# Kernel optimization log

Hardware: AMD Instinct MI355X
Metric: run time of the kernel (lower is better)

## Reference

```python
import jax, jax.numpy as jnp
import numpy as np

L = 2048   # input_len
D = 768    # d_model
K = 24     # num_eigh
K_U = 3    # auto_reg_k_u
K_Y = 2    # auto_reg_k_y


def get_top_hankel_eigh(n, k):
    # Hankel matrix Z[i,j] = 2 / ((i+j)^3 - (i+j)), 1-indexed
    i = np.arange(1, n + 1, dtype=np.float64)
    s = i[:, None] + i[None, :]
    z = 2.0 / (s ** 3 - s)
    vals, vecs = np.linalg.eigh(z)
    return (jnp.asarray(vals[-k:], jnp.float32),      # [k]
            jnp.asarray(vecs[:, -k:], jnp.float32))   # [n, k]


def setup_inputs() -> dict:
    key = jax.random.key(0)
    k1, k2, k3, k4 = jax.random.split(key, 4)
    inputs = jax.random.normal(k1, (L, D), jnp.float32)
    m_y = 0.01 * jax.random.normal(k2, (D, K_Y, D), jnp.float32)
    m_u = (1.0 / D ** 0.5) * jax.random.normal(k3, (D, D, K_U), jnp.float32)
    m_phi = 0.02 * jax.random.normal(k4, (D * K, D), jnp.float32)
    eig_vals, eig_vecs = get_top_hankel_eigh(L, K)
    return {"inputs": inputs, "m_y": m_y, "m_u": m_u, "m_phi": m_phi,
            "eig_vals": eig_vals, "eig_vecs": eig_vecs}


def _conv(v, u):
    # Causal (truncated) convolution of every filter with every channel via FFT.
    # v: [l, k] spectral filters, u: [l, d] inputs -> [l, k, d]
    l = v.shape[0]
    vf = jnp.fft.rfft(v, n=2 * l, axis=0)   # [l+1, k]
    uf = jnp.fft.rfft(u, n=2 * l, axis=0)   # [l+1, d]
    return jnp.fft.irfft(vf[:, :, None] * uf[:, None, :], n=2 * l, axis=0)[:l]


def _compute_x_tilde(inputs, eig_vals, eig_vecs, do_shift=True):
    l = inputs.shape[0]
    x = _conv(eig_vecs, inputs) * (eig_vals[None, :, None] ** 0.25)  # [l, k, d]
    x = x.reshape(l, -1)                                             # [l, k*d]
    if do_shift:
        # shift twice (zero-pad at front); the first two lags are handled by AR part
        x = jnp.pad(x, ((2, 0), (0, 0)))[:l]
    return x


def _compute_ar_x_preds(w, x):
    # w: [d_out, d_in, k_u], x: [l, d_in] -> [l, d_out]
    d_out, d_in, k = w.shape
    l = x.shape[0]
    o = jnp.einsum('oik,li->klo', w, x)                     # [k, l, d_out]
    o = jax.vmap(lambda a, s: jnp.roll(a, s, axis=0))(o, jnp.arange(k))
    m = jnp.triu(jnp.ones((k, l), dtype=x.dtype))[:, :, None]  # zero wrap-around
    return jnp.sum(o * m, axis=0)


def _compute_y_t(m_y, deltas):
    # y_t = sum_i m_y[:, i] @ y_{t-1-i} + delta_t, as a linear recurrence scan
    d_out, k, _ = m_y.shape

    def step(carry, x):                                 # carry: [k, d_out]
        out = jnp.tensordot(m_y, carry, axes=2) + x     # [d_out]
        carry = jnp.concatenate([out[None], carry[:-1]], axis=0)
        return carry, out

    _, ys = jax.lax.scan(step, jnp.zeros((k, d_out), deltas.dtype), deltas)
    return ys


def reference(inputs, m_y, m_u, m_phi, eig_vals, eig_vecs):
    x_tilde = _compute_x_tilde(inputs, eig_vals, eig_vecs, True)  # [l, k*d]
    delta_phi = x_tilde @ m_phi                                   # [l, d]
    delta_ar_u = _compute_ar_x_preds(m_u, inputs)                 # [l, d]
    return _compute_y_t(m_y, delta_phi + delta_ar_u)              # [l, d]
```

## Files before the change

kernel.cpp:

```cpp
#include <hip/hip_runtime.h>
#include <hip/hip_bf16.h>
#include <stdint.h>


typedef unsigned short u16;
typedef unsigned int   u32;
typedef __bf16  bf16x8 __attribute__((ext_vector_type(8)));
typedef float   f32x4  __attribute__((ext_vector_type(4)));
typedef u32     u32x4  __attribute__((ext_vector_type(4)));

#define MFMA(a,b,c) __builtin_amdgcn_mfma_f32_16x16x32_bf16(a,b,c,0,0,0)
#define RJ 1179648

__device__ __forceinline__ u16 f2b(float f) {
  union { float f; u32 u; } v; v.f = f;
  return (u16)((v.u + 0x7fffu + ((v.u >> 16) & 1u)) >> 16);
}

__device__ __forceinline__ void gld16(const u16* g, u16* l) {
  __builtin_amdgcn_global_load_lds(
      (const __attribute__((address_space(1))) u32*)g,
      (__attribute__((address_space(3))) u32*)l, 16, 0, 0);
}

#define WS_UB     0
#define WS_MPHIT  3148800
#define WS_B2T    31460352
#define WS_TT     34999296
#define WS_ZT     48368640
#define WS_DELTA  123866112
#define OV_RBIG   (WS_ZT + 0)
#define OV_CT0    (WS_ZT + 21233664)
#define OV_CT1    (WS_ZT + 25952256)
#define OV_CT2    (WS_ZT + 30670848)
#define OV_HBUF   (WS_ZT + 35389440)
#define OV_SBUF   (WS_ZT + 41680896)

__global__ void k_prep(const float* __restrict__ u, const float* __restrict__ mphi,
                       const float* __restrict__ ev, const float* __restrict__ mu,
                       const float* __restrict__ evec,
                       float* __restrict__ delta, u16* __restrict__ ub,
                       u16* __restrict__ mphiT, u16* __restrict__ b2t,
                       u16* __restrict__ tt) {
  __shared__ float tile[32][33];
  int b = blockIdx.x, tid = threadIdx.x;
  if (b < 6144) {
    delta[b * 256 + tid] = 0.f;
  } else if (b < 12294) {
    int i = (b - 6144) * 256 + tid;
    ub[i] = (i < 2 * 768) ? (u16)0 : f2b(u[i - 2 * 768]);
  } else if (b < 26118) {
    int bid = b - 12294;
    int k = bid / 576, rem = bid % 576;
    int ti = rem / 24, tj = rem % 24;
    int c = tid & 31, r0 = tid >> 5;
    float s = powf(ev[k], 0.25f);
    #pragma unroll
    for (int rr = 0; rr < 4; ++rr) {
      int r = r0 + (rr << 3);
      tile[r][c] = mphi[(k * 768 + ti * 32 + r) * 768 + tj * 32 + c];
    }
    __syncthreads();
    #pragma unroll
    for (int rr = 0; rr < 4; ++rr) {
      int r = r0 + (rr << 3);
      mphiT[(k * 768 + tj * 32 + r) * 768 + ti * 32 + c] = f2b(tile[c][r] * s);
    }
  } else if (b < 33030) {
    int i = (b - 26118) * 256 + tid;
    int kk = i / (768 * 768);
    int rem = i % (768 * 768);
    int o = rem / 768, ii = rem % 768;
    b2t[i] = f2b(mu[(o * 768 + ii) * 3 + kk]);
  } else {
    int i = (b - 33030) * 256 + tid;
    int c = i & 127, r = (i >> 7) & 127;
    int kk = (i >> 14) % 24, sl = (i >> 14) / 24;
    int t = (sl - 1) * 128 + r - c - 2;
    tt[i] = (t >= 0 && t < 2048) ? f2b(evec[t * 24 + kk]) : (u16)0;
  }
}

__device__ __forceinline__ void stage128(const u16* __restrict__ g, int ld,
                                         u16* __restrict__ lds) {
  int tid = threadIdx.x;
  int r0 = tid >> 3, cb = tid & 7, wave = tid >> 6;
  #pragma unroll
  for (int s = 0; s < 4; ++s) {
    int row = r0 + (s << 5);
    int cbx = (cb ^ (row & 7)) << 3;
    gld16(g + row * ld + cbx, lds + (s << 11) + (wave << 9));
  }
}

__device__ __forceinline__ void mfma_tile(const u16* As, const u16* Bs, int lane,
                                          int wm, int wn, f32x4 acc[4][4]) {
  int cn = lane & 15, q = lane >> 4;
  #pragma unroll
  for (int ks = 0; ks < 2; ++ks) {
    int blk = ks * 4 + q;
    bf16x8 af[4], bg[4];
    #pragma unroll
    for (int i = 0; i < 4; ++i) {
      int row = wm + i * 16 + cn;
      af[i] = *(const bf16x8*)&As[row * 64 + ((blk ^ (row & 7)) << 3)];
    }
    #pragma unroll
    for (int j = 0; j < 4; ++j) {
      int row = wn + j * 16 + cn;
      bg[j] = *(const bf16x8*)&Bs[row * 64 + ((blk ^ (row & 7)) << 3)];
    }
    #pragma unroll
    for (int i = 0; i < 4; ++i)
      #pragma unroll
      for (int j = 0; j < 4; ++j)
        acc[i][j] = MFMA(af[i], bg[j], acc[i][j]);
  }
}

__device__ __forceinline__ void mfma_tile256(const u16* As, const u16* Bs, int lane,
                                             int wm, f32x4 acc[4][8]) {
  int cn = lane & 15, q = lane >> 4;
  #pragma unroll
  for (int ks = 0; ks < 2; ++ks) {
    int blk = ks * 4 + q;
    bf16x8 af[4], bg[8];
    #pragma unroll
    for (int i = 0; i < 4; ++i) {
      int row = wm + i * 16 + cn;
      af[i] = *(const bf16x8*)&As[row * 64 + ((blk ^ (row & 7)) << 3)];
    }
    #pragma unroll
    for (int j = 0; j < 8; ++j) {
      int row = j * 16 + cn;
      bg[j] = *(const bf16x8*)&Bs[row * 64 + ((blk ^ (row & 7)) << 3)];
    }
    #pragma unroll
    for (int i = 0; i < 4; ++i)
      #pragma unroll
      for (int j = 0; j < 8; ++j)
        acc[i][j] = MFMA(af[i], bg[j], acc[i][j]);
  }
}

__global__ __launch_bounds__(256, 2) void k_gemm_zt(const u16* __restrict__ A,
                                                    const u16* __restrict__ B,
                                                    u16* __restrict__ C) {
  __shared__ __align__(16) u16 As[256 * 64];
  __shared__ __align__(16) u16 Bs[128 * 64];
  int bid = blockIdx.x;
  bid = (bid & 7) * 144 + (bid >> 3);
  int nt = bid & 15, mt = bid >> 4;
  int m0 = mt << 8, n0 = nt << 7;
  int tid = threadIdx.x, lane = tid & 63, wave = tid >> 6;
  int wm = wave << 6;
  f32x4 acc[4][8] = {};
  for (int kb = 0; kb < 12; ++kb) {
    stage128(A + m0 * 768 + kb * 64, 768, As);
    stage128(A + (m0 + 128) * 768 + kb * 64, 768, As + 8192);
    stage128(B + n0 * 768 + kb * 64, 768, Bs);
    __syncthreads();
    mfma_tile256(As, Bs, lane, wm, acc);
    __syncthreads();
  }
  int q = lane >> 4, cn = lane & 15;
  #pragma unroll
  for (int i = 0; i < 4; ++i)
    #pragma unroll
    for (int j = 0; j < 8; ++j)
      #pragma unroll
      for (int r = 0; r < 4; ++r) {
        int m = m0 + wm + i * 16 + q * 4 + r;
        int n = n0 + j * 16 + cn;
        C[m * 2048 + n] = f2b(acc[i][j][r]);
      }
}

__global__ __launch_bounds__(256, 2) void k_gemm_delta(const u16* __restrict__ tt,
                                                       const u16* __restrict__ zt,
                                                       const u16* __restrict__ ub,
                                                       const u16* __restrict__ b2t,
                                                       float* __restrict__ delta) {
  __shared__ __align__(16) u16 As[256 * 64];
  __shared__ __align__(16) u16 Bs[128 * 64];
  int bid = blockIdx.x;
  bid = (bid & 7) * 54 + (bid >> 3);
  int s = 0, rem = bid;
  for (;; ++s) { int c = 6 * (8 - (s >> 1)); if (rem < c) break; rem -= c; }
  int cnt = 8 - (s >> 1);
  int db = rem / cnt;
  int a  = (s >> 1) + rem % cnt;
  int n0 = db << 7;
  int tid = threadIdx.x, lane = tid & 63, wave = tid >> 6;
  int wm = wave << 6;
  f32x4 acc[4][8] = {};
  int d1 = 2 * a + 1 - s;
  const u16* A0 = tt + (size_t)d1 * 24 * 16384;
  const u16* A1 = tt + (size_t)(d1 + 1) * 24 * 16384;
  for (int kk = 0; kk < 24; ++kk) {
    const u16* Bg = zt + kk * (768 * 2048) + n0 * 2048 + s * 128;
    #pragma unroll
    for (int hf = 0; hf < 2; ++hf) {
      stage128(A0 + kk * 16384 + hf * 64, 128, As);
      stage128(A1 + kk * 16384 + hf * 64, 128, As + 8192);
      stage128(Bg + hf * 64, 2048, Bs);
      __syncthreads();
      mfma_tile256(As, Bs, lane, wm, acc);
      __syncthreads();
    }
  }
  #pragma unroll
  for (int kku = 0; kku < 3; ++kku) {
    int owner = (kku <= 2 * a + 1) ? kku : 2 * a + 1;
    if (s != owner) continue;
    const u16* Au = ub + (2 + a * 256 - kku) * 768;
    const u16* Bg = b2t + kku * (768 * 768) + n0 * 768;
    for (int ic = 0; ic < 12; ++ic) {
      stage128(Au + ic * 64, 768, As);
      stage128(Au + 128 * 768 + ic * 64, 768, As + 8192);
      stage128(Bg + ic * 64, 768, Bs);
      __syncthreads();
      mfma_tile256(As, Bs, lane, wm, acc);
      __syncthreads();
    }
  }
  int q = lane >> 4, cn = lane & 15;
  #pragma unroll
  for (int i = 0; i < 4; ++i)
    #pragma unroll
    for (int j = 0; j < 8; ++j)
      #pragma unroll
      for (int r = 0; r < 4; ++r) {
        int m = a * 256 + wm + i * 16 + q * 4 + r;
        int n = n0 + j * 16 + cn;
        unsafeAtomicAdd(&delta[m * 768 + n], acc[i][j][r]);
      }
}

__global__ void k_chain_init(const float* __restrict__ my, u16* __restrict__ Rbig,
                             u16* __restrict__ Ct0, u16* __restrict__ Ct1,
                             float* __restrict__ Hbuf) {
  int b = blockIdx.x, tid = threadIdx.x;
  if (b < 4608) {
    int i = b * 256 + tid;
    int o = i / 1536, q = i % 1536;
    Rbig[i] = (q == o) ? (u16)0x3F80 : (u16)0;
    Rbig[RJ + i] = f2b(my[i]);
  } else if (b < 13824) {
    int i = (b - 4608) * 256 + tid;
    int n = i / 1536, p = i % 1536;
    u16 v;
    if (p < 768) v = f2b(my[p * 1536 + n]);
    else         v = (p - 768 == n) ? (u16)0x3F80 : (u16)0;
    Ct0[i] = v;
  } else if (b < 18432) {
    int i = (b - 13824) * 256 + tid;
    int n = i / 768, ii = i % 768;
    Ct1[n * 1536 + 768 + ii] = f2b(my[ii * 1536 + n]);
  } else {
    int i = (b - 18432) * 256 + tid;
    Hbuf[i] = 0.f;
  }
}

__global__ __launch_bounds__(256) void k_gemm_R(const u16* __restrict__ A,
                                                const u16* __restrict__ Ct,
                                                u16* __restrict__ Co,
                                                u16* __restrict__ CtT, int mode) {
  __shared__ __align__(16) u16 As[128 * 64];
  __shared__ __align__(16) u16 Bs[128 * 64];
  int bid = blockIdx.x;
  int nt = bid % 12, mt = bid / 12;
  int m0 = mt << 7, n0 = nt << 7;
  int tid = threadIdx.x, lane = tid & 63, wave = tid >> 6;
  int wm = (wave & 1) << 6, wn = (wave >> 1) << 6;
  f32x4 acc[4][4] = {};
  for (int kb = 0; kb < 24; ++kb) {
    stage128(A + m0 * 1536 + kb * 64, 1536, As);
    stage128(Ct + n0 * 1536 + kb * 64, 1536, Bs);
    __syncthreads();
    mfma_tile(As, Bs, lane, wm, wn, acc);
    __syncthreads();
  }
  int q = lane >> 4, cn = lane & 15;
  #pragma unroll
  for (int i = 0; i < 4; ++i)
    #pragma unroll
    for (int j = 0; j < 4; ++j) {
      int n = n0 + wn + j * 16 + cn;
      int mb = m0 + wm + i * 16 + q * 4;
      u16 pk[4];
      #pragma unroll
      for (int r = 0; r < 4; ++r) {
        u16 v = f2b(acc[i][j][r]);
        Co[(mb + r) * 1536 + n] = v;
        pk[r] = v;
      }
      if (mode) {
        int tcol = (mode == 1) ? mb : ((mb < 768) ? 768 + mb : mb - 768);
        *(uint2*)&CtT[n * 1536 + tcol] = *(uint2*)pk;
      }
    }
}

__global__ __launch_bounds__(256) void k_conv(const float* __restrict__ delta,
                                              const u16* __restrict__ Rbig,
                                              float* __restrict__ Hbuf) {
  __shared__ __align__(16) u16 As[128 * 64];
  __shared__ __align__(16) u16 Bs[128 * 64];
  int bid = blockIdx.x;
  bid = (bid & 7) * 48 + (bid >> 3);
  int nt = bid % 6, mt = (bid / 6) % 16, sp = bid / 96;
  int m0 = mt << 7, n0 = nt << 7;
  int tid = threadIdx.x, lane = tid & 63, wave = tid >> 6;
  int wm = (wave & 1) << 6, wn = (wave >> 1) << 6;
  int trow = tid >> 3, cb = tid & 7;
  f32x4 acc[4][4] = {};
  for (int kb = 0; kb < 24; ++kb) {
    int i = 2 * sp + kb / 12, dinb = kb % 12;
    #pragma unroll
    for (int s = 0; s < 4; ++s) {
      int row = trow + (s << 5);
      int t = m0 + row;
      u16 pk[8] = {0, 0, 0, 0, 0, 0, 0, 0};
      if (i <= (t & 7)) {
        const float* src = delta + (t - i) * 768 + dinb * 64 + (cb << 3);
        f32x4 v0 = *(const f32x4*)src;
        f32x4 v1 = *(const f32x4*)(src + 4);
        #pragma unroll
        for (int e = 0; e < 4; ++e) { pk[e] = f2b(v0[e]); pk[4 + e] = f2b(v1[e]); }
      }
      *(u32x4*)&As[row * 64 + ((cb ^ (row & 7)) << 3)] = *(u32x4*)pk;
    }
    stage128(Rbig + i * RJ + n0 * 1536 + dinb * 64, 1536, Bs);
    __syncthreads();
    mfma_tile(As, Bs, lane, wm, wn, acc);
    __syncthreads();
  }
  int q = lane >> 4, cn = lane & 15;
  #pragma unroll
  for (int i = 0; i < 4; ++i)
    #pragma unroll
    for (int j = 0; j < 4; ++j)
      #pragma unroll
      for (int r = 0; r < 4; ++r) {
        int m = m0 + wm + i * 16 + q * 4 + r;
        int n = n0 + wn + j * 16 + cn;
        unsafeAtomicAdd(&Hbuf[m * 768 + n], acc[i][j][r]);
      }
}

__global__ __launch_bounds__(256) void k_scan_roundA(const u16* __restrict__ Rbig,
                                                     const float* __restrict__ Hbuf,
                                                     u16* __restrict__ Sout) {
  __shared__ __align__(16) u16 As[128 * 64];
  __shared__ __align__(16) u16 Bs[128 * 64];
  int bid = blockIdx.x;
  int nt = bid % 12, mt = bid / 12;
  int m0 = mt << 7, n0 = nt << 7;
  const u16* Bg = (nt < 6) ? (Rbig + 8 * RJ + n0 * 1536)
                           : (Rbig + 7 * RJ + (n0 - 768) * 1536);
  int tid = threadIdx.x, lane = tid & 63, wave = tid >> 6;
  int wm = (wave & 1) << 6, wn = (wave >> 1) << 6;
  int trow = tid >> 3, cb = tid & 7;
  f32x4 acc[4][4] = {};
  for (int kb = 0; kb < 24; ++kb) {
    #pragma unroll
    for (int s = 0; s < 4; ++s) {
      int row = trow + (s << 5);
      int c = m0 + row;
      int qb = kb * 64 + (cb << 3);
      int side = (qb >= 768) ? 1 : 0;
      int o0 = qb - side * 768;
      int t = 8 * c - 17 - side;
      u16 pk[8] = {0, 0, 0, 0, 0, 0, 0, 0};
      if (t >= 0) {
        const float* src = Hbuf + t * 768 + o0;
        f32x4 v0 = *(const f32x4*)src;
        f32x4 v1 = *(const f32x4*)(src + 4);
        #pragma unroll
        for (int e = 0; e < 4; ++e) { pk[e] = f2b(v0[e]); pk[4 + e] = f2b(v1[e]); }
      }
      *(u32x4*)&As[row * 64 + ((cb ^ (row & 7)) << 3)] = *(u32x4*)pk;
    }
    stage128(Bg + kb * 64, 1536, Bs);
    __syncthreads();
    mfma_tile(As, Bs, lane, wm, wn, acc);
    __syncthreads();
  }
  int q = lane >> 4, cn = lane & 15;
  #pragma unroll
  for (int i = 0; i < 4; ++i)
    #pragma unroll
    for (int j = 0; j < 4; ++j)
      #pragma unroll
      for (int r = 0; r < 4; ++r) {
        int c = m0 + wm + i * 16 + q * 4 + r;
        int n = n0 + wn + j * 16 + cn;
        int side = (n < 768) ? 0 : 1;
        int t = 8 * c - 9 - side;
        int o = n - side * 768;
        float val = acc[i][j][r] + ((t >= 0) ? Hbuf[t * 768 + o] : 0.f);
        Sout[c * 1536 + n] = f2b(val);
      }
}

__global__ __launch_bounds__(256) void k_scan_round(const u16* __restrict__ Sin,
                                                    const u16* __restrict__ Rbig,
                                                    const float* __restrict__ Hbuf,
                                                    u16* __restrict__ Sout) {
  __shared__ __align__(16) u16 As[128 * 64];
  __shared__ __align__(16) u16 Bs[128 * 64];
  int bid = blockIdx.x;
  int nt = bid % 12, mt = bid / 12;
  int m0 = mt << 7, n0 = nt << 7;
  const u16* Bg = (nt < 6) ? (Rbig + 8 * RJ + n0 * 1536)
                           : (Rbig + 7 * RJ + (n0 - 768) * 1536);
  int tid = threadIdx.x, lane = tid & 63, wave = tid >> 6;
  int wm = (wave & 1) << 6, wn = (wave >> 1) << 6;
  f32x4 acc[4][4] = {};
  for (int kb = 0; kb < 24; ++kb) {
    stage128(Sin + m0 * 1536 + kb * 64, 1536, As);
    stage128(Bg + kb * 64, 1536, Bs);
    __syncthreads();
    mfma_tile(As, Bs, lane, wm, wn, acc);
    __syncthreads();
  }
  int q = lane >> 4, cn = lane & 15;
  #pragma unroll
  for (int i = 0; i < 4; ++i)
    #pragma unroll
    for (int j = 0; j < 4; ++j)
      #pragma unroll
      for (int r = 0; r < 4; ++r) {
        int c = m0 + wm + i * 16 + q * 4 + r;
        int n = n0 + wn + j * 16 + cn;
        int side = (n < 768) ? 0 : 1;
        int t = 8 * c - 1 - side;
        int o = n - side * 768;
        float val = acc[i][j][r] + ((t >= 0) ? Hbuf[t * 768 + o] : 0.f);
        Sout[c * 1536 + n] = f2b(val);
      }
}

__global__ __launch_bounds__(256) void k_scan_out(const u16* __restrict__ Sin,
                                                  const u16* __restrict__ Rbig,
                                                  const float* __restrict__ Hbuf,
                                                  float* __restrict__ out) {
  __shared__ __align__(16) u16 As[128 * 64];
  __shared__ __align__(16) u16 Bs[128 * 64];
  int bid = blockIdx.x;
  int nt = bid % 48, mt = bid / 48;
  int m0 = mt << 7, n0 = nt << 7;
  const u16* Bg = Rbig + RJ + n0 * 1536;
  int tid = threadIdx.x, lane = tid & 63, wave = tid >> 6;
  int wm = (wave & 1) << 6, wn = (wave >> 1) << 6;
  f32x4 acc[4][4] = {};
  for (int kb = 0; kb < 24; ++kb) {
    stage128(Sin + m0 * 1536 + kb * 64, 1536, As);
    stage128(Bg + kb * 64, 1536, Bs);
    __syncthreads();
    mfma_tile(As, Bs, lane, wm, wn, acc);
    __syncthreads();
  }
  int q = lane >> 4, cn = lane & 15;
  #pragma unroll
  for (int i = 0; i < 4; ++i)
    #pragma unroll
    for (int j = 0; j < 4; ++j)
      #pragma unroll
      for (int r = 0; r < 4; ++r) {
        int c = m0 + wm + i * 16 + q * 4 + r;
        int n = n0 + wn + j * 16 + cn;
        int jj = n / 768, o = n % 768;
        int t = 8 * c + jj;
        out[t * 768 + o] = acc[i][j][r] + Hbuf[t * 768 + o];
      }
}

extern "C" void kernel_launch(void* const* d_in, const int* in_sizes, int n_in,
                              void* d_out, int out_size, void* d_ws, size_t ws_size,
                              hipStream_t stream) {
  const float* u    = (const float*)d_in[0];
  const float* my   = (const float*)d_in[1];
  const float* mu   = (const float*)d_in[2];
  const float* mphi = (const float*)d_in[3];
  const float* ev   = (const float*)d_in[4];
  const float* evec = (const float*)d_in[5];
  float* out = (float*)d_out;
  char* ws = (char*)d_ws;

  u16*   ub    = (u16*)(ws + WS_UB);
  u16*   mphiT = (u16*)(ws + WS_MPHIT);
  u16*   b2t   = (u16*)(ws + WS_B2T);
  u16*   tt    = (u16*)(ws + WS_TT);
  u16*   zt    = (u16*)(ws + WS_ZT);
  float* delta = (float*)(ws + WS_DELTA);
  u16*   Rbig  = (u16*)(ws + OV_RBIG);
  u16*   Ct0   = (u16*)(ws + OV_CT0);
  u16*   Ct1   = (u16*)(ws + OV_CT1);
  u16*   Ct2   = (u16*)(ws + OV_CT2);
  float* Hbuf  = (float*)(ws + OV_HBUF);
  u16*   SA    = (u16*)(ws + OV_SBUF);
  u16*   SB    = SA + 256 * 1536;

  hipLaunchKernelGGL(k_prep, dim3(59142), dim3(256), 0, stream,
                     u, mphi, ev, mu, evec, delta, ub, mphiT, b2t, tt);
  hipLaunchKernelGGL(k_gemm_zt,    dim3(1152), dim3(256), 0, stream,
                     mphiT, ub + 2 * 768, zt);
  hipLaunchKernelGGL(k_gemm_delta, dim3(432),  dim3(256), 0, stream,
                     tt, zt, ub, b2t, delta);

  hipLaunchKernelGGL(k_chain_init, dim3(24576), dim3(256), 0, stream,
                     my, Rbig, Ct0, Ct1, Hbuf);
  hipLaunchKernelGGL(k_gemm_R, dim3(72),  dim3(256), 0, stream,
                     Rbig + RJ, Ct0, Rbig + 2 * RJ, Ct1, 1);
  hipLaunchKernelGGL(k_gemm_R, dim3(144), dim3(256), 0, stream,
                     Rbig + RJ, Ct1, Rbig + 3 * RJ, Ct2, 2);
  hipLaunchKernelGGL(k_gemm_R, dim3(288), dim3(256), 0, stream,
                     Rbig + RJ, Ct2, Rbig + 5 * RJ, (u16*)nullptr, 0);

  hipLaunchKernelGGL(k_conv, dim3(384), dim3(256), 0, stream, delta, Rbig, Hbuf);

  hipLaunchKernelGGL(k_scan_roundA, dim3(24), dim3(256), 0, stream, Rbig, Hbuf, SA);
  hipLaunchKernelGGL(k_scan_round,  dim3(24), dim3(256), 0, stream, SA, Rbig, Hbuf, SB);
  hipLaunchKernelGGL(k_scan_out,    dim3(96), dim3(256), 0, stream, SB, Rbig, Hbuf, out);
}
```

Before: 625.9 us.

## Double-buffer LDS staging in zt and delta GEMMs to overlap loads with MFMA

Both GEMM kernels now keep two LDS buffers and issue the global-to-LDS loads for the next k-slab before running the MFMA tile on the current one, with one waitcnt-plus-barrier per slab instead of two syncthreads. The delta kernel's spectral and AR-tap loops are merged into a single slab sequence so the pipeline runs across both phases. LDS use doubles, so launch bounds drop to one block per CU, trading occupancy for overlap of memory latency with compute.

```diff
diff --git a/kernel.cpp b/kernel.cpp
--- a/kernel.cpp
+++ b/kernel.cpp
@@ -21,6 +21,12 @@
   __builtin_amdgcn_global_load_lds(
       (const __attribute__((address_space(1))) u32*)g,
       (__attribute__((address_space(3))) u32*)l, 16, 0, 0);
+}
+
+__device__ __forceinline__ void pipe_sync() {
+  asm volatile("s_waitcnt vmcnt(0)" ::: "memory");
+  __builtin_amdgcn_s_barrier();
+  __builtin_amdgcn_sched_barrier(0);
 }
 
 #define WS_UB     0
@@ -143,11 +149,11 @@
   }
 }
 
-__global__ __launch_bounds__(256, 2) void k_gemm_zt(const u16* __restrict__ A,
+__global__ __launch_bounds__(256, 1) void k_gemm_zt(const u16* __restrict__ A,
                                                     const u16* __restrict__ B,
                                                     u16* __restrict__ C) {
-  __shared__ __align__(16) u16 As[256 * 64];
-  __shared__ __align__(16) u16 Bs[128 * 64];
+  __shared__ __align__(16) u16 As[2 * 256 * 64];
+  __shared__ __align__(16) u16 Bs[2 * 128 * 64];
   int bid = blockIdx.x;
   bid = (bid & 7) * 144 + (bid >> 3);
   int nt = bid & 15, mt = bid >> 4;
@@ -155,13 +161,23 @@
   int tid = threadIdx.x, lane = tid & 63, wave = tid >> 6;
   int wm = wave << 6;
   f32x4 acc[4][8] = {};
+
+  auto STAGE = [&](int kb, int half) {
+    u16* Ad = As + half * (256 * 64);
+    u16* Bd = Bs + half * (128 * 64);
+    stage128(A + m0 * 768 + kb * 64, 768, Ad);
+    stage128(A + (m0 + 128) * 768 + kb * 64, 768, Ad + 8192);
+    stage128(B + n0 * 768 + kb * 64, 768, Bd);
+  };
+
+  STAGE(0, 0);
+  pipe_sync();
+  int cur = 0;
   for (int kb = 0; kb < 12; ++kb) {
-    stage128(A + m0 * 768 + kb * 64, 768, As);
-    stage128(A + (m0 + 128) * 768 + kb * 64, 768, As + 8192);
-    stage128(B + n0 * 768 + kb * 64, 768, Bs);
-    __syncthreads();
-    mfma_tile256(As, Bs, lane, wm, acc);
-    __syncthreads();
+    if (kb + 1 < 12) STAGE(kb + 1, cur ^ 1);
+    mfma_tile256(As + cur * (256 * 64), Bs + cur * (128 * 64), lane, wm, acc);
+    if (kb + 1 < 12) pipe_sync();
+    cur ^= 1;
   }
   int q = lane >> 4, cn = lane & 15;
   #pragma unroll
@@ -176,13 +192,13 @@
       }
 }
 
-__global__ __launch_bounds__(256, 2) void k_gemm_delta(const u16* __restrict__ tt,
+__global__ __launch_bounds__(256, 1) void k_gemm_delta(const u16* __restrict__ tt,
                                                        const u16* __restrict__ zt,
                                                        const u16* __restrict__ ub,
                                                        const u16* __restrict__ b2t,
                                                        float* __restrict__ delta) {
-  __shared__ __align__(16) u16 As[256 * 64];
-  __shared__ __align__(16) u16 Bs[128 * 64];
+  __shared__ __align__(16) u16 As[2 * 256 * 64];
+  __shared__ __align__(16) u16 Bs[2 * 128 * 64];
   int bid = blockIdx.x;
   bid = (bid & 7) * 54 + (bid >> 3);
   int s = 0, rem = bid;
@@ -197,32 +213,37 @@
   int d1 = 2 * a + 1 - s;
   const u16* A0 = tt + (size_t)d1 * 24 * 16384;
   const u16* A1 = tt + (size_t)(d1 + 1) * 24 * 16384;
-  for (int kk = 0; kk < 24; ++kk) {
-    const u16* Bg = zt + kk * (768 * 2048) + n0 * 2048 + s * 128;
-    #pragma unroll
-    for (int hf = 0; hf < 2; ++hf) {
-      stage128(A0 + kk * 16384 + hf * 64, 128, As);
-      stage128(A1 + kk * 16384 + hf * 64, 128, As + 8192);
-      stage128(Bg + hf * 64, 2048, Bs);
-      __syncthreads();
-      mfma_tile256(As, Bs, lane, wm, acc);
-      __syncthreads();
-    }
-  }
-  #pragma unroll
-  for (int kku = 0; kku < 3; ++kku) {
-    int owner = (kku <= 2 * a + 1) ? kku : 2 * a + 1;
-    if (s != owner) continue;
-    const u16* Au = ub + (2 + a * 256 - kku) * 768;
-    const u16* Bg = b2t + kku * (768 * 768) + n0 * 768;
-    for (int ic = 0; ic < 12; ++ic) {
-      stage128(Au + ic * 64, 768, As);
-      stage128(Au + 128 * 768 + ic * 64, 768, As + 8192);
-      stage128(Bg + ic * 64, 768, Bs);
-      __syncthreads();
-      mfma_tile256(As, Bs, lane, wm, acc);
-      __syncthreads();
-    }
+  const u16* ztb = zt + n0 * 2048 + s * 128;
+  int ntaps = (s > 2) ? 0 : ((s == 2 * a + 1) ? (3 - s) : 1);
+  int nslab = 48 + 12 * ntaps;
+
+  auto STAGE = [&](int t, int half) {
+    u16* Ad = As + half * (256 * 64);
+    u16* Bd = Bs + half * (128 * 64);
+    if (t < 48) {
+      int kk = t >> 1, hf = t & 1;
+      stage128(A0 + kk * 16384 + hf * 64, 128, Ad);
+      stage128(A1 + kk * 16384 + hf * 64, 128, Ad + 8192);
+      stage128(ztb + kk * (768 * 2048) + hf * 64, 2048, Bd);
+    } else {
+      int ti = t - 48;
+      int kku = s + ti / 12;
+      int ic = ti % 12;
+      const u16* Au = ub + (2 + a * 256 - kku) * 768;
+      stage128(Au + ic * 64, 768, Ad);
+      stage128(Au + 128 * 768 + ic * 64, 768, Ad + 8192);
+      stage128(b2t + kku * (768 * 768) + n0 * 768 + ic * 64, 768, Bd);
+    }
+  };
+
+  STAGE(0, 0);
+  pipe_sync();
+  int cur = 0;
+  for (int t = 0; t < nslab; ++t) {
+    if (t + 1 < nslab) STAGE(t + 1, cur ^ 1);
+    mfma_tile256(As + cur * (256 * 64), Bs + cur * (128 * 64), lane, wm, acc);
+    if (t + 1 < nslab) pipe_sync();
+    cur ^= 1;
   }
   int q = lane >> 4, cn = lane & 15;
   #pragma unroll
```

After: 777.9 us. +24.3%, slower.
